# Optimization experiments

Measured on AMD Instinct MI355X. Metric: run time of the kernel, lower is better.

Reference implementation:

```python
import jax, jax.numpy as jnp
import numpy as np

SHIFTS = [1, 2, 4]  # matches init_kwargs 'shifts' (all in range 0 < s < channels)


def setup_inputs() -> dict:
    key = jax.random.key(0)
    k1, k2, k3 = jax.random.split(key, 3)
    B, H, L, D = 4, 1, 2048, 512
    factor = 4
    proj_in = 2 * len(SHIFTS) * D  # cli_mode='full' -> 2 components per shift
    x = jax.random.normal(k1, (B, H, L, D), dtype=jnp.float32)
    W = jax.random.normal(k2, (factor, D), dtype=jnp.float32) * 0.05
    # glorot-ish scale for the projection kernel
    proj_kernel = jax.random.normal(k3, (proj_in, D), dtype=jnp.float32) * (1.0 / np.sqrt(proj_in))
    proj_bias = jnp.zeros((D,), dtype=jnp.float32)
    return {"x": x, "W": W, "proj_kernel": proj_kernel, "proj_bias": proj_bias}


def reference(x, W, proj_kernel, proj_bias):
    # x: (B, H, L, D); W: (k, D) slot multivectors
    k, D = W.shape
    B, H, L, _ = x.shape
    # coarse[-1] treated as zeros; non-anchor slots source previous coarse vector
    coarse_prev = jnp.pad(x, ((0, 0), (0, 0), (1, 0), (0, 0)))[:, :, :-1, :]
    # src: (B, H, L, k, D) — slots 0..k-2 from coarse_prev, slot k-1 (anchor) from x
    src = jnp.concatenate(
        [jnp.repeat(coarse_prev[:, :, :, None, :], k - 1, axis=3),
         x[:, :, :, None, :]],
        axis=3,
    )
    W_b = W[None, None, None, :, :]  # (1,1,1,k,D)
    components = []
    for s in SHIFTS:
        src_s = jnp.roll(src, s, axis=-1)
        W_s_b = jnp.roll(W, s, axis=-1)[None, None, None, :, :]
        sw = src * W_s_b
        components.append(sw - W_b * src_s)        # wedge part
        components.append(jax.nn.silu(sw))          # inner part (full mode)
    g = jnp.concatenate(components, axis=-1)  # (B,H,L,k, 2*len(shifts)*D)
    fine = jnp.einsum('bhlkc,cd->bhlkd', g, proj_kernel) + proj_bias
    return fine.reshape(B, H, L * k, D)
```

## Files before the change

kernel.cpp:

```cpp
#include <hip/hip_runtime.h>
#include <cstdint>
#include <cstddef>

#define D_DIM 512
#define L_DIM 2048
#define KB_DIM 2048
#define KS_DIM 1536
#define NROWS_X 2049
#define M_TOT 32768

typedef __bf16 bf16x8 __attribute__((ext_vector_type(8)));
typedef float  f32x4  __attribute__((ext_vector_type(4)));

__device__ __forceinline__ unsigned f2bf(float f) {
  unsigned u = __float_as_uint(f);
  u += 0x7FFF + ((u >> 16) & 1);
  return u >> 16;
}
__device__ __forceinline__ float bf2f(unsigned short u) {
  return __uint_as_float(((unsigned)u) << 16);
}
__device__ __forceinline__ void gld_lds16(const void* g, void* l) {
  __builtin_amdgcn_global_load_lds((const __attribute__((address_space(1))) void*)g,
                                   (__attribute__((address_space(3))) void*)l,
                                   16, 0, 0);
}

__global__ __launch_bounds__(256) void prep(
    const float* __restrict__ x, const float* __restrict__ W, const float* __restrict__ P,
    unsigned short* __restrict__ XbfZ, unsigned short* __restrict__ Ball,
    unsigned short* __restrict__ GS, int doGS) {
  __shared__ unsigned short WtabL[6144];
  const int tid = threadIdx.x;

  if (blockIdx.x < 2048) {
    for (int i = tid; i < 6144; i += 256) {
      const int c = i & 511; const int rest = i >> 9;
      const int si = rest % 3; const int jj = rest / 3;
      WtabL[i] = (unsigned short)f2bf(W[jj * 512 + ((c - (1 << si)) & 511)]);
    }
    __syncthreads();

    const int r = tid >> 6, lane = tid & 63;
    const int gr = blockIdx.x * 4 + r;
    const int b = gr >> 11, l = gr & 2047;

    const float4* xr = reinterpret_cast<const float4*>(x) + ((size_t)(b * L_DIM + l)) * 128 + lane * 2;
    const float4 v0 = xr[0], v1 = xr[1];
    union U { uint4 q; unsigned short s[8]; };
    U va;
    va.q.x = f2bf(v0.x) | (f2bf(v0.y) << 16);
    va.q.y = f2bf(v0.z) | (f2bf(v0.w) << 16);
    va.q.z = f2bf(v1.x) | (f2bf(v1.y) << 16);
    va.q.w = f2bf(v1.z) | (f2bf(v1.w) << 16);
    *reinterpret_cast<uint4*>(XbfZ + ((size_t)(b * NROWS_X + l + 1)) * 512 + lane * 8) = va.q;

    if (doGS) {
      #pragma unroll
      for (int j = 0; j < 4; ++j) {
        const int lam = (j < 3) ? (l + 1) : l;
        const bool wr = (j == 3) || (l < 2047);
        unsigned short* o = GS + ((size_t)((j * 4 + b) * L_DIM + lam)) * KS_DIM + lane * 8;
        #pragma unroll
        for (int si = 0; si < 3; ++si) {
          U wa;
          wa.q = *reinterpret_cast<const uint4*>(&WtabL[(j * 3 + si) * 512 + lane * 8]);
          unsigned res[4];
          #pragma unroll
          for (int e = 0; e < 4; ++e) {
            float s0 = bf2f(va.s[2 * e])     * bf2f(wa.s[2 * e]);
            float s1 = bf2f(va.s[2 * e + 1]) * bf2f(wa.s[2 * e + 1]);
            float g0 = s0 * __builtin_amdgcn_rcpf(1.f + __expf(-s0));
            float g1 = s1 * __builtin_amdgcn_rcpf(1.f + __expf(-s1));
            res[e] = f2bf(g0) | (f2bf(g1) << 16);
          }
          if (wr) {
            uint4 ov = {res[0], res[1], res[2], res[3]};
            *reinterpret_cast<uint4*>(o + si * 512) = ov;
          }
        }
      }
    }
    if (l == 2047) {
      const uint4 z = {0u, 0u, 0u, 0u};
      *reinterpret_cast<uint4*>(XbfZ + ((size_t)(b * NROWS_X)) * 512 + lane * 8) = z;
      if (doGS) {
        #pragma unroll
        for (int j = 0; j < 3; ++j)
          #pragma unroll
          for (int si = 0; si < 3; ++si)
            *reinterpret_cast<uint4*>(GS + ((size_t)((j * 4 + b) * L_DIM)) * KS_DIM + si * 512 + lane * 8) = z;
      }
    }
    return;
  }

  const int bx = blockIdx.x - 2048;
  const int j = bx >> 6, dt = (bx >> 3) & 7, ct = bx & 7;
  const int d = dt * 64 + (tid & 63);
  const int cbase = ct * 64 + (tid >> 6) * 16;
  unsigned short bufd[16];
  unsigned short bufs[3][16];
  #pragma unroll
  for (int cc = 0; cc < 16; ++cc) {
    const int c = cbase + cc;
    float qd = 0.f;
    #pragma unroll
    for (int si = 0; si < 3; ++si) {
      const int s = 1 << si;
      const int cm = (c - s) & 511, cp = (c + s) & 511;
      qd += W[j * 512 + cm] * P[((size_t)(2 * si) * 512 + c) * 512 + d]
          - W[j * 512 + cp] * P[((size_t)(2 * si) * 512 + cp) * 512 + d];
      bufs[si][cc] = (unsigned short)f2bf(P[((size_t)(2 * si + 1) * 512 + c) * 512 + d]);
    }
    bufd[cc] = (unsigned short)f2bf(qd);
  }
  unsigned short* row = Ball + (size_t)(j * 512 + d) * KB_DIM;
  *reinterpret_cast<uint4*>(&row[cbase])     = *reinterpret_cast<uint4*>(&bufd[0]);
  *reinterpret_cast<uint4*>(&row[cbase + 8]) = *reinterpret_cast<uint4*>(&bufd[8]);
  #pragma unroll
  for (int si = 0; si < 3; ++si) {
    *reinterpret_cast<uint4*>(&row[512 + si * 512 + cbase])     = *reinterpret_cast<uint4*>(&bufs[si][0]);
    *reinterpret_cast<uint4*>(&row[512 + si * 512 + cbase + 8]) = *reinterpret_cast<uint4*>(&bufs[si][8]);
  }
}

#define BARR asm volatile("s_barrier" ::: "memory")
#define VMW(N) asm volatile("s_waitcnt vmcnt(" #N ")" ::: "memory")

__global__ __launch_bounds__(256, 3) void gemm128(
    const unsigned short* __restrict__ XbfZ, const unsigned short* __restrict__ GS,
    const unsigned short* __restrict__ Ball, const float* __restrict__ bias,
    float* __restrict__ out) {
  __shared__ alignas(16) unsigned short A_lds[3][4096];
  __shared__ alignas(16) unsigned short B_lds[3][4096];

  const int tid = threadIdx.x;
  const int bid = blockIdx.x;
  const int wid = (bid & 7) * 128 + (bid >> 3);
  const int mtile = wid >> 2;
  const int ntile = wid & 3;
  const int j  = mtile >> 6;
  const int b  = (mtile >> 4) & 3;
  const int l0 = (mtile & 15) * 128;
  const int n0 = ntile * 128;
  const size_t mbase = (size_t)((j * 4 + b) * L_DIM + l0);

  const int srow = tid >> 2;
  const int spos = tid & 3;
  const int sc   = spos ^ (srow & 3) ^ ((srow >> 2) & 3);
  const unsigned short* pXd = XbfZ + ((size_t)(b * NROWS_X + (j == 3) + l0 + srow)) * 512 + sc * 8;
  const unsigned short* pGS = GS + (mbase + srow) * (size_t)KS_DIM + sc * 8;
  const unsigned short* pB  = Ball + ((size_t)(j * 512 + n0 + srow)) * KB_DIM + sc * 8;
  const int ldsSlot = tid * 8;

  auto stageA = [&](int TT, int bufi) {
    unsigned short* dst = &A_lds[bufi][ldsSlot];
    if (TT < 16) {
      const unsigned short* s = pXd + TT * 32;
      gld_lds16(s, dst);
      gld_lds16(s + 64 * 512, dst + 2048);
    } else {
      const unsigned short* s = pGS + (TT - 16) * 32;
      gld_lds16(s, dst);
      gld_lds16(s + 64 * KS_DIM, dst + 2048);
    }
  };
  auto stageB = [&](int TT, int bufi) {
    const unsigned short* s = pB + TT * 32;
    unsigned short* dst = &B_lds[bufi][ldsSlot];
    gld_lds16(s, dst);
    gld_lds16(s + 64 * KB_DIM, dst + 2048);
  };

  const int lane = tid & 63, wv = tid >> 6;
  const int wm = wv >> 1, wn = wv & 1;
  const int l16 = lane & 15, quad = lane >> 4;
  const int rp = (quad ^ (l16 & 3) ^ ((l16 >> 2) & 3)) * 8;
  int aOff[4], bOff[4];
  #pragma unroll
  for (int mf = 0; mf < 4; ++mf) aOff[mf] = (wm * 64 + mf * 16 + l16) * 32 + rp;
  #pragma unroll
  for (int nf = 0; nf < 4; ++nf) bOff[nf] = (wn * 64 + nf * 16 + l16) * 32 + rp;

  f32x4 acc[4][4];
  #pragma unroll
  for (int i = 0; i < 4; ++i)
    #pragma unroll
    for (int n = 0; n < 4; ++n)
      acc[i][n] = f32x4{0.f, 0.f, 0.f, 0.f};

  bf16x8 a[4], bf[4];

  stageA(0, 0); stageB(0, 0);
  stageA(1, 1); stageB(1, 1);
  VMW(4);
  BARR;

  int cur = 0;
  for (int T = 0; T < 64; ++T) {
    const int rs = (cur >= 1) ? (cur - 1) : 2;
    if (T + 2 < 64) { stageA(T + 2, rs); stageB(T + 2, rs); }
    const unsigned short* Ac = A_lds[cur];
    const unsigned short* Bc = B_lds[cur];
    #pragma unroll
    for (int mf = 0; mf < 4; ++mf)
      a[mf] = __builtin_bit_cast(bf16x8, *reinterpret_cast<const uint4*>(&Ac[aOff[mf]]));
    #pragma unroll
    for (int nf = 0; nf < 4; ++nf)
      bf[nf] = __builtin_bit_cast(bf16x8, *reinterpret_cast<const uint4*>(&Bc[bOff[nf]]));
    __builtin_amdgcn_s_setprio(1);
    #pragma unroll
    for (int mf = 0; mf < 4; ++mf)
      #pragma unroll
      for (int nf = 0; nf < 4; ++nf)
        acc[mf][nf] = __builtin_amdgcn_mfma_f32_16x16x32_bf16(a[mf], bf[nf], acc[mf][nf], 0, 0, 0);
    __builtin_amdgcn_s_setprio(0);
    if (T < 62) {
      VMW(4);
      BARR;
    } else if (T == 62) {
      VMW(0);
      BARR;
    }
    cur = (cur >= 2) ? 0 : (cur + 1);
  }

  #pragma unroll
  for (int nf = 0; nf < 4; ++nf) {
    const int d = n0 + wn * 64 + nf * 16 + l16;
    const float bv = bias[d];
    #pragma unroll
    for (int mf = 0; mf < 4; ++mf) {
      const int lrow = l0 + wm * 64 + mf * 16 + quad * 4;
      #pragma unroll
      for (int rg = 0; rg < 4; ++rg) {
        out[((size_t)(b * L_DIM + lrow + rg) * 4 + j) * D_DIM + d] = acc[mf][nf][rg] + bv;
      }
    }
  }
}

__global__ __launch_bounds__(256, 2) void fused_gemm(
    const unsigned short* __restrict__ XbfZ, const unsigned short* __restrict__ Ball,
    const float* __restrict__ W, const float* __restrict__ bias,
    float* __restrict__ out) {
  __shared__ alignas(16) unsigned short Vt[2][4096];
  __shared__ alignas(16) unsigned short Bt[2][8192];
  __shared__ alignas(16) unsigned short At[128 * 40];
  __shared__ alignas(16) unsigned short Wr[3 * 512];

  const int tid = threadIdx.x;
  const int nt = blockIdx.x & 1;
  const int mt = blockIdx.x >> 1;
  const int j  = mt >> 6;
  const int b  = (mt >> 4) & 3;
  const int lt = mt & 15;
  const int l0 = lt * 128;
  const int n0 = nt * 256;
  const int base_l = l0 - ((j == 3) ? 0 : 1);

  #pragma unroll
  for (int i = 0; i < 6; ++i) {
    const int idx = tid + i * 256;
    const int si = idx >> 9, c = idx & 511, s = 1 << si;
    Wr[idx] = (unsigned short)f2bf(W[j * 512 + ((c - s) & 511)]);
  }

  const int lane = tid & 63, wv = tid >> 6;
  const int qv = (lane & 3) ^ ((lane >> 4) & 3);
  const int rsub = lane >> 2;
  const unsigned short* gA0 = XbfZ + ((size_t)(b * NROWS_X + 1 + base_l + (wv * 2) * 16 + rsub)) * 512 + qv * 8;
  const unsigned short* gA1 = gA0 + (size_t)16 * 512;
  const unsigned short* gB[4];
  #pragma unroll
  for (int pi = 0; pi < 4; ++pi)
    gB[pi] = Ball + (size_t)(j * 512 + n0 + (wv * 4 + pi) * 16 + rsub) * KB_DIM + qv * 8;
  const int vOff0 = wv * 1024 + lane * 8;
  const int bOff0 = wv * 2048 + lane * 8;

  const int am = tid >> 1;
  const int akh = (tid & 1) * 16;
  const int ch0 = (tid & 1) * 2;
  const int sswz = (am >> 2) & 3;
  unsigned short* aDst = &At[am * 40 + akh];

  const int l16 = lane & 15, quad = lane >> 4;
  const int wm = wv >> 1, wn = wv & 1;
  const int fsw = (l16 >> 2) & 3;
  const int aVoff = (wm * 64 + l16) * 32 + ((quad ^ fsw)) * 8;
  const int aSoff = (wm * 64 + l16) * 40 + quad * 8;
  const int bOffF = (wn * 128 + l16) * 32 + ((quad ^ fsw)) * 8;

  f32x4 acc[4][8];
  #pragma unroll
  for (int i = 0; i < 4; ++i)
    #pragma unroll
    for (int n = 0; n < 8; ++n)
      acc[i][n] = f32x4{0.f, 0.f, 0.f, 0.f};

  {
    gld_lds16(gA0, &Vt[0][vOff0]);
    gld_lds16(gA1, &Vt[0][vOff0 + 512]);
    #pragma unroll
    for (int pi = 0; pi < 4; ++pi)
      gld_lds16(gB[pi], &Bt[0][bOff0 + pi * 512]);
  }

  for (int it = 0; it < 64; ++it) {
    const int buf = it & 1;
    const int kk0 = it * 32;
    const int gi = kk0 >> 9;

    __syncthreads();

    if (it + 1 < 64) {
      const int nk = kk0 + 32;
      const int nv = nk & 511;
      gld_lds16(gA0 + nv, &Vt[buf ^ 1][vOff0]);
      gld_lds16(gA1 + nv, &Vt[buf ^ 1][vOff0 + 512]);
      #pragma unroll
      for (int pi = 0; pi < 4; ++pi)
        gld_lds16(gB[pi] + nk, &Bt[buf ^ 1][bOff0 + pi * 512]);
    }

    bf16x8 af[4], bfr[8];
    if (gi == 0) {
      #pragma unroll
      for (int mi = 0; mi < 4; ++mi) {
        uint4 r = *reinterpret_cast<const uint4*>(&Vt[buf][aVoff + mi * 512]);
        af[mi] = __builtin_bit_cast(bf16x8, r);
      }
    } else {
      const int si = gi - 1;
      const int ccbase = (kk0 & 511) + akh;
      uint4 v0 = *reinterpret_cast<const uint4*>(&Vt[buf][(am * 4 + ((ch0)     ^ sswz)) * 8]);
      uint4 v1 = *reinterpret_cast<const uint4*>(&Vt[buf][(am * 4 + ((ch0 + 1) ^ sswz)) * 8]);
      uint4 w0 = *reinterpret_cast<const uint4*>(&Wr[si * 512 + ccbase]);
      uint4 w1 = *reinterpret_cast<const uint4*>(&Wr[si * 512 + ccbase + 8]);
      union U { uint4 q[2]; unsigned short s[16]; };
      U va, wa; va.q[0] = v0; va.q[1] = v1; wa.q[0] = w0; wa.q[1] = w1;
      unsigned res[8];
      #pragma unroll
      for (int e = 0; e < 8; ++e) {
        float s0 = bf2f(va.s[2 * e])     * bf2f(wa.s[2 * e]);
        float s1 = bf2f(va.s[2 * e + 1]) * bf2f(wa.s[2 * e + 1]);
        float g0 = s0 * __builtin_amdgcn_rcpf(1.f + __expf(-s0));
        float g1 = s1 * __builtin_amdgcn_rcpf(1.f + __expf(-s1));
        res[e] = f2bf(g0) | (f2bf(g1) << 16);
      }
      uint4 o0 = {res[0], res[1], res[2], res[3]};
      uint4 o1 = {res[4], res[5], res[6], res[7]};
      *reinterpret_cast<uint4*>(aDst) = o0;
      *reinterpret_cast<uint4*>(aDst + 8) = o1;
      __syncthreads();
      #pragma unroll
      for (int mi = 0; mi < 4; ++mi) {
        uint4 r = *reinterpret_cast<const uint4*>(&At[aSoff + mi * 640]);
        af[mi] = __builtin_bit_cast(bf16x8, r);
      }
    }
    #pragma unroll
    for (int ni = 0; ni < 8; ++ni) {
      uint4 r = *reinterpret_cast<const uint4*>(&Bt[buf][bOffF + ni * 512]);
      bfr[ni] = __builtin_bit_cast(bf16x8, r);
    }
    #pragma unroll
    for (int mi = 0; mi < 4; ++mi)
      #pragma unroll
      for (int ni = 0; ni < 8; ++ni)
        acc[mi][ni] = __builtin_amdgcn_mfma_f32_16x16x32_bf16(af[mi], bfr[ni], acc[mi][ni], 0, 0, 0);
  }

  #pragma unroll
  for (int ni = 0; ni < 8; ++ni) {
    const int d = n0 + wn * 128 + ni * 16 + l16;
    const float bv = bias[d];
    #pragma unroll
    for (int mi = 0; mi < 4; ++mi) {
      const int lrow = l0 + wm * 64 + mi * 16 + quad * 4;
      #pragma unroll
      for (int rg = 0; rg < 4; ++rg) {
        out[((size_t)(b * L_DIM + lrow + rg) * 4 + j) * D_DIM + d] = acc[mi][ni][rg] + bv;
      }
    }
  }
}

extern "C" void kernel_launch(void* const* d_in, const int* in_sizes, int n_in,
                              void* d_out, int out_size, void* d_ws, size_t ws_size,
                              hipStream_t stream) {
  const float* x    = (const float*)d_in[0];
  const float* W    = (const float*)d_in[1];
  const float* P    = (const float*)d_in[2];
  const float* bias = (const float*)d_in[3];
  float* out = (float*)d_out;

  unsigned short* XbfZ = (unsigned short*)d_ws;
  unsigned short* Ball = XbfZ + (size_t)4 * NROWS_X * 512;
  unsigned short* GS   = Ball + (size_t)4 * 512 * KB_DIM + 6144;
  const size_t need_bytes =
      ((size_t)4 * NROWS_X * 512 + (size_t)4 * 512 * KB_DIM + 6144 +
       (size_t)M_TOT * KS_DIM) * 2;
  const bool primary = ws_size >= need_bytes;

  prep<<<2304, 256, 0, stream>>>(x, W, P, XbfZ, Ball, GS, primary ? 1 : 0);
  if (primary) {
    gemm128<<<dim3(1024), dim3(256), 0, stream>>>(XbfZ, GS, Ball, bias, out);
  } else {
    fused_gemm<<<512, 256, 0, stream>>>(XbfZ, Ball, W, bias, out);
  }
}
```

Measured before the change: 206.7 us.

## Switch GEMM to double-buffered LDS with pair-row swizzle and higher occupancy

Replaces the triple-buffered, two-stage-ahead prefetch, which used manual vmcnt waits and barriers, with a double buffer that prefetches one stage ahead and ends each iteration with __syncthreads. The LDS layout changes to pack row pairs into 64-element lines with an 8-way XOR swizzle, so reads should avoid bank conflicts. Launch bounds rise from 3 to 4 blocks per CU. The smaller LDS footprint buys occupancy, at the cost of less prefetch depth and a full drain at every barrier, since __syncthreads waits on all outstanding loads.

```diff
diff --git a/kernel.cpp b/kernel.cpp
--- a/kernel.cpp
+++ b/kernel.cpp
@@ -125,15 +125,12 @@
   }
 }
 
-#define BARR asm volatile("s_barrier" ::: "memory")
-#define VMW(N) asm volatile("s_waitcnt vmcnt(" #N ")" ::: "memory")
-
-__global__ __launch_bounds__(256, 3) void gemm128(
+__global__ __launch_bounds__(256, 4) void gemm128b(
     const unsigned short* __restrict__ XbfZ, const unsigned short* __restrict__ GS,
     const unsigned short* __restrict__ Ball, const float* __restrict__ bias,
     float* __restrict__ out) {
-  __shared__ alignas(16) unsigned short A_lds[3][4096];
-  __shared__ alignas(16) unsigned short B_lds[3][4096];
+  __shared__ alignas(16) unsigned short A_lds[2][4096];
+  __shared__ alignas(16) unsigned short B_lds[2][4096];
 
   const int tid = threadIdx.x;
   const int bid = blockIdx.x;
@@ -146,9 +143,11 @@
   const int n0 = ntile * 128;
   const size_t mbase = (size_t)((j * 4 + b) * L_DIM + l0);
 
-  const int srow = tid >> 2;
-  const int spos = tid & 3;
-  const int sc   = spos ^ (srow & 3) ^ ((srow >> 2) & 3);
+  const int pIdx = tid >> 3;
+  const int spos = tid & 7;
+  const int q    = spos ^ (pIdx & 7);
+  const int sc   = q >> 1;
+  const int srow = pIdx * 2 + (q & 1);
   const unsigned short* pXd = XbfZ + ((size_t)(b * NROWS_X + (j == 3) + l0 + srow)) * 512 + sc * 8;
   const unsigned short* pGS = GS + (mbase + srow) * (size_t)KS_DIM + sc * 8;
   const unsigned short* pB  = Ball + ((size_t)(j * 512 + n0 + srow)) * KB_DIM + sc * 8;
@@ -176,12 +175,13 @@
   const int lane = tid & 63, wv = tid >> 6;
   const int wm = wv >> 1, wn = wv & 1;
   const int l16 = lane & 15, quad = lane >> 4;
-  const int rp = (quad ^ (l16 & 3) ^ ((l16 >> 2) & 3)) * 8;
+  const int rp = (((quad << 1) | (l16 & 1)) ^ ((l16 >> 1) & 7)) * 8;
+  const int rpair = (l16 >> 1) * 64;
   int aOff[4], bOff[4];
   #pragma unroll
-  for (int mf = 0; mf < 4; ++mf) aOff[mf] = (wm * 64 + mf * 16 + l16) * 32 + rp;
-  #pragma unroll
-  for (int nf = 0; nf < 4; ++nf) bOff[nf] = (wn * 64 + nf * 16 + l16) * 32 + rp;
+  for (int mf = 0; mf < 4; ++mf) aOff[mf] = (wm * 32 + mf * 8) * 64 + rpair + rp;
+  #pragma unroll
+  for (int nf = 0; nf < 4; ++nf) bOff[nf] = (wn * 32 + nf * 8) * 64 + rpair + rp;
 
   f32x4 acc[4][4];
   #pragma unroll
@@ -193,16 +193,13 @@
   bf16x8 a[4], bf[4];
 
   stageA(0, 0); stageB(0, 0);
-  stageA(1, 1); stageB(1, 1);
-  VMW(4);
-  BARR;
-
-  int cur = 0;
+  __syncthreads();
+
   for (int T = 0; T < 64; ++T) {
-    const int rs = (cur >= 1) ? (cur - 1) : 2;
-    if (T + 2 < 64) { stageA(T + 2, rs); stageB(T + 2, rs); }
-    const unsigned short* Ac = A_lds[cur];
-    const unsigned short* Bc = B_lds[cur];
+    const int buf = T & 1;
+    if (T + 1 < 64) { stageA(T + 1, buf ^ 1); stageB(T + 1, buf ^ 1); }
+    const unsigned short* Ac = A_lds[buf];
+    const unsigned short* Bc = B_lds[buf];
     #pragma unroll
     for (int mf = 0; mf < 4; ++mf)
       a[mf] = __builtin_bit_cast(bf16x8, *reinterpret_cast<const uint4*>(&Ac[aOff[mf]]));
@@ -216,14 +213,7 @@
       for (int nf = 0; nf < 4; ++nf)
         acc[mf][nf] = __builtin_amdgcn_mfma_f32_16x16x32_bf16(a[mf], bf[nf], acc[mf][nf], 0, 0, 0);
     __builtin_amdgcn_s_setprio(0);
-    if (T < 62) {
-      VMW(4);
-      BARR;
-    } else if (T == 62) {
-      VMW(0);
-      BARR;
-    }
-    cur = (cur >= 2) ? 0 : (cur + 1);
+    __syncthreads();
   }
 
   #pragma unroll
@@ -406,7 +396,7 @@
 
   prep<<<2304, 256, 0, stream>>>(x, W, P, XbfZ, Ball, GS, primary ? 1 : 0);
   if (primary) {
-    gemm128<<<dim3(1024), dim3(256), 0, stream>>>(XbfZ, GS, Ball, bias, out);
+    gemm128b<<<dim3(1024), dim3(256), 0, stream>>>(XbfZ, GS, Ball, bias, out);
   } else {
     fused_gemm<<<512, 256, 0, stream>>>(XbfZ, Ball, W, bias, out);
   }
```

After: 190.7 us. 1.08x faster.
